# Kernel tuning notes

Measured on AMD Instinct MI355X. Metric: run time of the kernel, lower is better.

## Reference

```python
import jax, jax.numpy as jnp
import numpy as np

N_TV_ITER = 20      # fixed Chambolle iteration count (skimage early-stops via eps; fixed for jit)
TV_WEIGHT = 0.1


def _div(p):
    # negative adjoint of forward-difference gradient (skimage convention)
    d = -(p[0] + p[1])
    d = d.at[1:, :].add(p[0, :-1, :])
    d = d.at[:, 1:].add(p[1, :, :-1])
    return d


def tv_chambolle_2d(image):
    """skimage.restoration.denoise_tv_chambolle on a single 2D image, weight=0.1."""
    tau = 0.25  # 1 / (2 * ndim)

    def step(p, _):
        out = image + _div(p)
        gy = jnp.zeros_like(out).at[:-1, :].set(out[1:, :] - out[:-1, :])
        gx = jnp.zeros_like(out).at[:, :-1].set(out[:, 1:] - out[:, :-1])
        norm = jnp.sqrt(gy * gy + gx * gx)
        g = jnp.stack([gy, gx])
        p = (p - tau * g) / (1.0 + (tau / TV_WEIGHT) * norm)
        return p, None

    p0 = jnp.zeros((2,) + image.shape, image.dtype)
    p, _ = jax.lax.scan(step, p0, None, length=N_TV_ITER)
    return image + _div(p)


def tv_denoise(img):  # [B,C,H,W], vmapped over B*C (replaces the CPU python loop)
    B, C, H, W = img.shape
    out = jax.vmap(tv_chambolle_2d)(img.reshape(B * C, H, W))
    return out.reshape(B, C, H, W)


def conv(x, w, stride=1, groups=1):
    pad = w.shape[2] // 2  # 'same'-style padding for odd kernels, 0 for 1x1
    return jax.lax.conv_general_dilated(
        x, w, (stride, stride), [(pad, pad), (pad, pad)],
        dimension_numbers=('NCHW', 'OIHW', 'NCHW'),
        feature_group_count=groups)


def haar_ll(x):
    # one level of pywt wavedec2('haar') LL band: 0.5 * sum over each 2x2 block
    return 0.5 * (x[..., ::2, ::2] + x[..., ::2, 1::2] + x[..., 1::2, ::2] + x[..., 1::2, 1::2])


def backbone(x, stem_w, dw_pw):
    # stride-32, 1280-channel EfficientNet-B0-style feature extractor
    x = jax.nn.silu(conv(x, stem_w, stride=2))
    for dw, pw in dw_pw:
        x = jax.nn.silu(conv(x, dw, stride=2, groups=dw.shape[0]))
        x = jax.nn.silu(conv(x, pw))
    return x


def setup_inputs() -> dict:
    key = jax.random.key(0)
    ks = jax.random.split(key, 16)
    B, H, W = 4, 512, 512

    def w(k, o, i, kh, kw):
        return jax.random.normal(k, (o, i, kh, kw), jnp.float32) * (1.0 / np.sqrt(i * kh * kw))

    return {
        "img": jax.random.normal(ks[0], (B, 1, H, W), jnp.float32),
        "stem_w": w(ks[1], 32, 1, 3, 3),
        "dw1_w": w(ks[2], 32, 1, 3, 3),  "pw1_w": w(ks[3], 64, 32, 1, 1),
        "dw2_w": w(ks[4], 64, 1, 3, 3),  "pw2_w": w(ks[5], 128, 64, 1, 1),
        "dw3_w": w(ks[6], 128, 1, 3, 3), "pw3_w": w(ks[7], 256, 128, 1, 1),
        "dw4_w": w(ks[8], 256, 1, 3, 3), "pw4_w": w(ks[9], 512, 256, 1, 1),
        "head_w": w(ks[10], 1280, 512, 1, 1),
        "proj_w": w(ks[11], 64, 1280, 1, 1),
        "proj_b": jnp.zeros((64,), jnp.float32),
        "final_w": w(ks[12], 1, 64, 1, 1),
        "final_b": jnp.zeros((1,), jnp.float32),
    }


def reference(img, stem_w, dw1_w, pw1_w, dw2_w, pw2_w, dw3_w, pw3_w, dw4_w, pw4_w,
              head_w, proj_w, proj_b, final_w, final_b):
    B, C, H, W = img.shape
    x = tv_denoise(img)                                     # fused TV Chambolle
    x = backbone(x, stem_w, [(dw1_w, pw1_w), (dw2_w, pw2_w), (dw3_w, pw3_w), (dw4_w, pw4_w)])
    x = jax.nn.silu(conv(x, head_w))                        # [B,1280,H/32,W/32]
    x = conv(x, proj_w) + proj_b[None, :, None, None]       # [B,64,H/32,W/32]
    x = jax.image.resize(x, (B, 64, H, W), method='bilinear')  # align_corners=False semantics
    ll = haar_ll(haar_ll(x))                                # 2-level Haar LL: [B,64,H/4,W/4]
    out = conv(ll, final_w) + final_b[None, :, None, None]  # [B,1,H/4,W/4]
    return out
```

## Files before the change

kernel.cpp:

```cpp
#include <hip/hip_runtime.h>
#include <math.h>

constexpr int BATCH = 4;
constexpr int IMG_H = 512, IMG_W = 512;
constexpr int IMG_HW = IMG_H * IMG_W;
constexpr int PSTR = BATCH * IMG_HW;

constexpr size_t O_PA   = 0;
constexpr size_t O_PB   = O_PA + 2 * (size_t)PSTR;
constexpr size_t O_DEN  = O_PB + 2 * (size_t)PSTR;
constexpr size_t O_A1   = O_DEN + (size_t)PSTR;
constexpr size_t O_A2   = O_A1 + 8388608;
constexpr size_t O_WT1  = O_A2 + 2097152;
constexpr size_t O_WT2  = O_WT1 + 32 * 64;
constexpr size_t O_WT3  = O_WT2 + 64 * 128;
constexpr size_t O_WT4  = O_WT3 + 128 * 256;
constexpr size_t O_WTH  = O_WT4 + 256 * 512;
constexpr size_t O_WCOMB= O_WTH + 512 * 1280;
constexpr size_t O_BCOMB= O_WCOMB + 1280;
constexpr size_t O_S    = O_BCOMB + 4;
constexpr size_t WS_FLOATS = O_S + 1024;

__device__ __forceinline__ float silu_f(float x) {
    return x / (1.0f + expf(-x));
}
__device__ __forceinline__ int clampi(int v, int lo, int hi) {
    return v < lo ? lo : (v > hi ? hi : v);
}

template <int NST, bool FIRST, bool LAST>
__global__ __launch_bounds__(512) void tv_reg(const float* __restrict__ img,
                                              const float* __restrict__ pin,
                                              float* __restrict__ pout) {
    constexpr int ROWS = 7, NW = 8, HL = 10, TC = 44, TR = 32;
    __shared__ float bndP[512], bndO[512];
    const int tid = threadIdx.x;
    const int lane = tid & 63, w = tid >> 6;
    const int b = blockIdx.z;
    const int r0 = blockIdx.y * TR, c0 = blockIdx.x * TC;
    const int gj = c0 - HL + lane;
    const int gjc = clampi(gj, 0, 511);
    const int gib = r0 - HL + w * ROWS;
    const float* I = img + b * IMG_HW;
    const bool interior = (r0 - HL >= 1) && (r0 + NW * ROWS - HL <= 511) &&
                          (c0 - HL >= 1) && (c0 + 64 - HL <= 511);

    float rim[ROWS], rp0[ROWS], rp1[ROWS], ro[ROWS];
#pragma unroll
    for (int k = 0; k < ROWS; ++k) {
        int gi = clampi(gib + k, 0, 511);
        rim[k] = I[(gi << 9) + gjc];
    }
    if (!FIRST) {
        const float* P0 = pin + b * IMG_HW;
        const float* P1 = pin + PSTR + b * IMG_HW;
#pragma unroll
        for (int k = 0; k < ROWS; ++k) {
            int gi = clampi(gib + k, 0, 511);
            rp0[k] = P0[(gi << 9) + gjc];
            rp1[k] = P1[(gi << 9) + gjc];
        }
    }
    const bool gjpos = (gj > 0), gjlt = (gj < 511);

    int s0 = 0;
    if (FIRST) {
        bndO[tid] = rim[0];
        __syncthreads();
        float odn = (w < NW - 1) ? bndO[tid + 64] : 0.0f;
        if (interior) {
#pragma unroll
            for (int k = 0; k < ROWS; ++k) {
                float oR = __shfl_down(rim[k], 1);
                float od = (k < ROWS - 1) ? rim[k + 1] : odn;
                float gy = od - rim[k];
                float gx = oR - rim[k];
                float inv = 1.0f / (1.0f + 2.5f * sqrtf(gy * gy + gx * gx));
                rp0[k] = -0.25f * gy * inv;
                rp1[k] = -0.25f * gx * inv;
            }
        } else {
#pragma unroll
            for (int k = 0; k < ROWS; ++k) {
                float oR = __shfl_down(rim[k], 1);
                float od = (k < ROWS - 1) ? rim[k + 1] : odn;
                int gi = gib + k;
                float gy = (gi < 511) ? od - rim[k] : 0.0f;
                float gx = gjlt ? oR - rim[k] : 0.0f;
                float inv = 1.0f / (1.0f + 2.5f * sqrtf(gy * gy + gx * gx));
                rp0[k] = -0.25f * gy * inv;
                rp1[k] = -0.25f * gx * inv;
            }
        }
        s0 = 1;
    }

    for (int s = s0; s < NST; ++s) {
        __syncthreads();
        bndP[tid] = rp0[ROWS - 1];
        __syncthreads();
        float pup0 = (w > 0) ? bndP[tid - 64] : 0.0f;
        if (interior) {
#pragma unroll
            for (int k = 0; k < ROWS; ++k) {
                float p1l = __shfl_up(rp1[k], 1);
                float pup = (k > 0) ? rp0[k - 1] : pup0;
                ro[k] = rim[k] - rp0[k] - rp1[k] + pup + p1l;
            }
            bndO[tid] = ro[0];
            __syncthreads();
            float odn = (w < NW - 1) ? bndO[tid + 64] : 0.0f;
#pragma unroll
            for (int k = 0; k < ROWS; ++k) {
                float oR = __shfl_down(ro[k], 1);
                float od = (k < ROWS - 1) ? ro[k + 1] : odn;
                float gy = od - ro[k];
                float gx = oR - ro[k];
                float inv = 1.0f / (1.0f + 2.5f * sqrtf(gy * gy + gx * gx));
                rp0[k] = (rp0[k] - 0.25f * gy) * inv;
                rp1[k] = (rp1[k] - 0.25f * gx) * inv;
            }
        } else {
#pragma unroll
            for (int k = 0; k < ROWS; ++k) {
                float p1l = __shfl_up(rp1[k], 1);
                float o = rim[k] - rp0[k] - rp1[k];
                float pup = (k > 0) ? rp0[k - 1] : pup0;
                int gi = gib + k;
                if (gi > 0) o += pup;
                if (gjpos) o += p1l;
                ro[k] = o;
            }
            bndO[tid] = ro[0];
            __syncthreads();
            float odn = (w < NW - 1) ? bndO[tid + 64] : 0.0f;
#pragma unroll
            for (int k = 0; k < ROWS; ++k) {
                float oR = __shfl_down(ro[k], 1);
                float od = (k < ROWS - 1) ? ro[k + 1] : odn;
                int gi = gib + k;
                float gy = (gi < 511) ? od - ro[k] : 0.0f;
                float gx = gjlt ? oR - ro[k] : 0.0f;
                float inv = 1.0f / (1.0f + 2.5f * sqrtf(gy * gy + gx * gx));
                rp0[k] = (rp0[k] - 0.25f * gy) * inv;
                rp1[k] = (rp1[k] - 0.25f * gx) * inv;
            }
        }
    }

    const bool cst = (lane >= HL && lane < HL + TC && gj < 512);
    if (LAST) {
        __syncthreads();
        bndP[tid] = rp0[ROWS - 1];
        __syncthreads();
        float pup0 = (w > 0) ? bndP[tid - 64] : 0.0f;
        float* D = pout + b * IMG_HW;
#pragma unroll
        for (int k = 0; k < ROWS; ++k) {
            float p1l = __shfl_up(rp1[k], 1);
            int gi = gib + k;
            int rk = w * ROWS + k;
            float o = rim[k] - rp0[k] - rp1[k];
            float pup = (k > 0) ? rp0[k - 1] : pup0;
            if (gi > 0) o += pup;
            if (gjpos) o += p1l;
            if (rk >= HL && rk < HL + TR && cst) D[(gi << 9) + gj] = o;
        }
    } else {
        float* Q0 = pout + b * IMG_HW;
        float* Q1 = pout + PSTR + b * IMG_HW;
#pragma unroll
        for (int k = 0; k < ROWS; ++k) {
            int rk = w * ROWS + k;
            int gi = gib + k;
            if (rk >= HL && rk < HL + TR && cst) {
                Q0[(gi << 9) + gj] = rp0[k];
                Q1[(gi << 9) + gj] = rp1[k];
            }
        }
    }
}

__global__ __launch_bounds__(256) void stem_dw1_pw1(const float* __restrict__ den,
                                                    const float* __restrict__ stemw,
                                                    const float* __restrict__ dw1w,
                                                    const float* __restrict__ pw1T,
                                                    float* __restrict__ out) {
    __shared__ float sDen[35 * 36];
    __shared__ float sStem[8 * 323];
    __shared__ float sDw[32 * 64];
    __shared__ float sW[576];
    __shared__ __align__(16) float sWp[2048];
    const int tid = threadIdx.x;
    const int b = blockIdx.z;
    const int r0 = blockIdx.y * 32, c0 = blockIdx.x * 32;
    const float* D = den + b * IMG_HW;
    for (int e = tid; e < 576; e += 256) sW[e] = (e < 288) ? stemw[e] : dw1w[e - 288];
    for (int e = tid; e < 2048; e += 256) sWp[e] = pw1T[e];
    for (int e = tid; e < 35 * 35; e += 256) {
        int li = e / 35, lj = e % 35;
        int gi = r0 - 3 + li, gjj = c0 - 3 + lj;
        sDen[li * 36 + lj] = (gi >= 0 && gjj >= 0) ? D[(gi << 9) + gjj] : 0.0f;
    }
    __syncthreads();

    for (int g = 0; g < 4; ++g) {
        if (g) __syncthreads();
        for (int e = tid; e < 2312; e += 256) {
            int pos = e >> 3, cl = e & 7;
            int sy = pos / 17, sx = pos % 17;
            int c = 8 * g + cl;
            const float* wc = &sW[c * 9];
            const float* dbase = &sDen[(2 * sy) * 36 + 2 * sx];
            float a = 0.0f;
#pragma unroll
            for (int ky = 0; ky < 3; ++ky)
#pragma unroll
                for (int kx = 0; kx < 3; ++kx)
                    a = fmaf(wc[ky * 3 + kx], dbase[ky * 36 + kx], a);
            sStem[cl * 323 + sy * 19 + sx] = silu_f(a);
        }
        __syncthreads();
        for (int e = tid; e < 512; e += 256) {
            int cl = e >> 6, dy = (e >> 3) & 7, dx = e & 7;
            int c = 8 * g + cl;
            float acc = 0.0f;
#pragma unroll
            for (int ky = 0; ky < 3; ++ky)
#pragma unroll
                for (int kx = 0; kx < 3; ++kx) {
                    int sgy = (r0 >> 1) - 1 + 2 * dy + ky;
                    int sgx = (c0 >> 1) - 1 + 2 * dx + kx;
                    float v = (sgy >= 0 && sgx >= 0)
                        ? sStem[cl * 323 + (2 * dy + ky) * 19 + 2 * dx + kx] : 0.0f;
                    acc = fmaf(sW[288 + c * 9 + ky * 3 + kx], v, acc);
                }
            sDw[c * 64 + (dy << 3) + dx] = silu_f(acc);
        }
    }
    __syncthreads();

    const int px = tid & 63, oc0 = (tid >> 6) * 16;
    float acc[16];
#pragma unroll
    for (int j = 0; j < 16; ++j) acc[j] = 0.0f;
    for (int ic = 0; ic < 32; ++ic) {
        float v = sDw[ic * 64 + px];
        const float* wr = &sWp[ic * 64 + oc0];
#pragma unroll
        for (int q = 0; q < 4; ++q) {
            float4 w4 = *(const float4*)(wr + q * 4);
            acc[q * 4 + 0] = fmaf(v, w4.x, acc[q * 4 + 0]);
            acc[q * 4 + 1] = fmaf(v, w4.y, acc[q * 4 + 1]);
            acc[q * 4 + 2] = fmaf(v, w4.z, acc[q * 4 + 2]);
            acc[q * 4 + 3] = fmaf(v, w4.w, acc[q * 4 + 3]);
        }
    }
    const int gpos = ((r0 >> 2) + (px >> 3)) * 128 + (c0 >> 2) + (px & 7);
    float* ob = out + (size_t)b * 64 * 16384 + (size_t)oc0 * 16384 + gpos;
#pragma unroll
    for (int j = 0; j < 16; ++j) ob[(size_t)j * 16384] = silu_f(acc[j]);
}

template <int C, int HIN>
__global__ __launch_bounds__(256) void dw_kernel(const float* __restrict__ in,
                                                 const float* __restrict__ w,
                                                 float* __restrict__ out) {
    constexpr int HO = HIN / 2;
    int t = blockIdx.x * 256 + threadIdx.x;
    int x = t % HO;
    int y = (t / HO) % HO;
    int c = (t / (HO * HO)) % C;
    int b = t / (HO * HO * C);
    const float* I = in + ((size_t)(b * C + c)) * (HIN * HIN);
    const float* wc = w + c * 9;
    int iy = 2 * y - 1, ix = 2 * x - 1;
    float acc = 0.0f;
#pragma unroll
    for (int ky = 0; ky < 3; ++ky)
#pragma unroll
        for (int kx = 0; kx < 3; ++kx) {
            int yy = iy + ky, xx = ix + kx;
            float vv = (yy >= 0 && xx >= 0) ? I[yy * HIN + xx] : 0.0f;
            acc = fmaf(wc[ky * 3 + kx], vv, acc);
        }
    out[t] = silu_f(acc);
}

template <int C, int HIN>
__global__ __launch_bounds__(256) void dw_reduce2_kernel(const float* __restrict__ part,
                                                         const float* __restrict__ w,
                                                         float* __restrict__ out) {
    constexpr int HO = HIN / 2;
    int t = blockIdx.x * 256 + threadIdx.x;
    int x = t % HO;
    int y = (t / HO) % HO;
    int c = (t / (HO * HO)) % C;
    int b = t / (HO * HO * C);
    const float* Ia = part + ((size_t)(b * C + c)) * (HIN * HIN);
    const float* Ib = Ia + (size_t)BATCH * C * HIN * HIN;
    const float* wc = w + c * 9;
    int iy = 2 * y - 1, ix = 2 * x - 1;
    float acc = 0.0f;
#pragma unroll
    for (int ky = 0; ky < 3; ++ky)
#pragma unroll
        for (int kx = 0; kx < 3; ++kx) {
            int yy = iy + ky, xx = ix + kx;
            float vv = 0.0f;
            if (yy >= 0 && xx >= 0) {
                int o = yy * HIN + xx;
                vv = silu_f(Ia[o] + Ib[o]);
            }
            acc = fmaf(wc[ky * 3 + kx], vv, acc);
        }
    out[t] = silu_f(acc);
}

template <int ICT, int NSIN, int NSPLIT, int OC, bool SILU>
__global__ __launch_bounds__(256) void pw_gemm(const float* __restrict__ in,
                                               const float* __restrict__ wT,
                                               float* __restrict__ out,
                                               int HW) {
    constexpr int KC = 32, TP = 64, TOC = 64, OPT = 4, PPT = 4;
    constexpr int KS = ICT / NSPLIT;
    constexpr int NC = KS / KC;
    constexpr int NOG = TOC / OPT;
    constexpr int PV4 = KC * TP / 4 / 256;
    constexpr int WV4 = KC * TOC / 4 / 256;
    static_assert(KS % KC == 0, "split");
    __shared__ __align__(16) float sPx[2][KC * TP];
    __shared__ __align__(16) float sW[2][KC * TOC];
    const int tid = threadIdx.x;
    const int zb = blockIdx.z;
    const int b = zb / NSPLIT, ks = zb % NSPLIT;
    const int p0 = blockIdx.x * TP;
    const int oc0 = blockIdx.y * TOC;
    const int ocg = tid % NOG, pxg = tid / NOG;
    const size_t instride = (size_t)BATCH * ICT * HW;
    const float* gin0 = in + ((size_t)b * ICT + ks * KS) * HW + p0;
    const float* gw0  = wT + ((size_t)(ks * KS)) * OC + oc0;

    float4 rp[PV4], rw[WV4];
    auto load_chunk = [&](int cc) {
        const float* gin = gin0 + (size_t)cc * KC * HW;
#pragma unroll
        for (int i = 0; i < PV4; ++i) {
            int e = tid + i * 256;
            int row = e / (TP / 4), col = e % (TP / 4);
            const float* base = gin + (size_t)row * HW + col * 4;
            float4 a = *(const float4*)base;
#pragma unroll
            for (int s = 1; s < NSIN; ++s) {
                float4 t4 = *(const float4*)(base + (size_t)s * instride);
                a.x += t4.x; a.y += t4.y; a.z += t4.z; a.w += t4.w;
            }
            if (NSIN > 1) {
                a.x = silu_f(a.x); a.y = silu_f(a.y);
                a.z = silu_f(a.z); a.w = silu_f(a.w);
            }
            rp[i] = a;
        }
        const float* gw = gw0 + (size_t)cc * KC * OC;
#pragma unroll
        for (int i = 0; i < WV4; ++i) {
            int e = tid + i * 256;
            int row = e / (TOC / 4), col = e % (TOC / 4);
            rw[i] = *(const float4*)(gw + (size_t)row * OC + col * 4);
        }
    };
    auto store_chunk = [&](int buf) {
#pragma unroll
        for (int i = 0; i < PV4; ++i) ((float4*)sPx[buf])[tid + i * 256] = rp[i];
#pragma unroll
        for (int i = 0; i < WV4; ++i) ((float4*)sW[buf])[tid + i * 256] = rw[i];
    };

    float acc[OPT][PPT];
#pragma unroll
    for (int o = 0; o < OPT; ++o)
#pragma unroll
        for (int p = 0; p < PPT; ++p) acc[o][p] = 0.0f;

    load_chunk(0);
    store_chunk(0);
    __syncthreads();
    for (int cc = 0; cc < NC; ++cc) {
        if (cc + 1 < NC) load_chunk(cc + 1);
        const int buf = cc & 1;
#pragma unroll 4
        for (int k = 0; k < KC; ++k) {
            float4 pv = *(const float4*)&sPx[buf][k * TP + pxg * PPT];
            float4 wv = *(const float4*)&sW[buf][k * TOC + ocg * OPT];
            float w0 = wv.x, w1 = wv.y, w2 = wv.z, w3 = wv.w;
            acc[0][0] = fmaf(pv.x, w0, acc[0][0]);
            acc[0][1] = fmaf(pv.y, w0, acc[0][1]);
            acc[0][2] = fmaf(pv.z, w0, acc[0][2]);
            acc[0][3] = fmaf(pv.w, w0, acc[0][3]);
            acc[1][0] = fmaf(pv.x, w1, acc[1][0]);
            acc[1][1] = fmaf(pv.y, w1, acc[1][1]);
            acc[1][2] = fmaf(pv.z, w1, acc[1][2]);
            acc[1][3] = fmaf(pv.w, w1, acc[1][3]);
            acc[2][0] = fmaf(pv.x, w2, acc[2][0]);
            acc[2][1] = fmaf(pv.y, w2, acc[2][1]);
            acc[2][2] = fmaf(pv.z, w2, acc[2][2]);
            acc[2][3] = fmaf(pv.w, w2, acc[2][3]);
            acc[3][0] = fmaf(pv.x, w3, acc[3][0]);
            acc[3][1] = fmaf(pv.y, w3, acc[3][1]);
            acc[3][2] = fmaf(pv.z, w3, acc[3][2]);
            acc[3][3] = fmaf(pv.w, w3, acc[3][3]);
        }
        if (cc + 1 < NC) {
            store_chunk((cc + 1) & 1);
            __syncthreads();
        }
    }

    float* ob;
    if (NSPLIT == 1)
        ob = out + ((size_t)(b * OC + oc0 + ocg * OPT)) * HW + p0 + pxg * PPT;
    else
        ob = out + (((size_t)(ks * BATCH + b)) * OC + oc0 + ocg * OPT) * HW + p0 + pxg * PPT;
#pragma unroll
    for (int o = 0; o < OPT; ++o) {
        float4 r;
        r.x = SILU ? silu_f(acc[o][0]) : acc[o][0];
        r.y = SILU ? silu_f(acc[o][1]) : acc[o][1];
        r.z = SILU ? silu_f(acc[o][2]) : acc[o][2];
        r.w = SILU ? silu_f(acc[o][3]) : acc[o][3];
        *(float4*)(ob + (size_t)o * HW) = r;
    }
}

__global__ __launch_bounds__(256) void prep_kernel(const float* __restrict__ pw1,
                                                   const float* __restrict__ pw2,
                                                   const float* __restrict__ pw3,
                                                   const float* __restrict__ pw4,
                                                   const float* __restrict__ headw,
                                                   const float* __restrict__ projw,
                                                   const float* __restrict__ projb,
                                                   const float* __restrict__ finalw,
                                                   const float* __restrict__ finalb,
                                                   float* __restrict__ ws) {
    int t = blockIdx.x * 256 + threadIdx.x;
    if (t < 2048) {
        int e = t; int ic = e >> 6, oc = e & 63;
        ws[O_WT1 + e] = pw1[oc * 32 + ic];
    } else if (t < 10240) {
        int e = t - 2048; int ic = e >> 7, oc = e & 127;
        ws[O_WT2 + e] = pw2[oc * 64 + ic];
    } else if (t < 43008) {
        int e = t - 10240; int ic = e >> 8, oc = e & 255;
        ws[O_WT3 + e] = pw3[oc * 128 + ic];
    } else if (t < 174080) {
        int e = t - 43008; int ic = e >> 9, oc = e & 511;
        ws[O_WT4 + e] = pw4[oc * 256 + ic];
    } else if (t < 829440) {
        int e = t - 174080; int ic = e / 1280, oc = e % 1280;
        ws[O_WTH + e] = headw[oc * 512 + ic];
    } else if (t < 830720) {
        int k = t - 829440;
        float a = 0.0f;
        for (int ch = 0; ch < 64; ++ch) a = fmaf(finalw[ch], projw[ch * 1280 + k], a);
        ws[O_WCOMB + k] = a;
    } else if (t == 830720) {
        float a = 0.0f;
        for (int ch = 0; ch < 64; ++ch) a = fmaf(finalw[ch], projb[ch], a);
        ws[O_BCOMB] = a;
    }
}

__global__ __launch_bounds__(256) void tail_head(const float* __restrict__ part,
                                                 const float* __restrict__ wcomb,
                                                 const float* __restrict__ bcomb,
                                                 float* __restrict__ s) {
    __shared__ float red[256];
    constexpr size_t PS = (size_t)4 * 1280 * 256;
    int b = blockIdx.x >> 4;
    int px0 = (blockIdx.x & 15) << 4;
    int px = threadIdx.x & 15, kg = threadIdx.x >> 4;
    const float* h0 = part + (size_t)b * 1280 * 256 + px0 + px;
    float acc = 0.0f;
    int k0 = kg * 80;
    for (int k = k0; k < k0 + 80; ++k) {
        size_t off = (size_t)k * 256;
        float v = silu_f(h0[off] + h0[off + PS] + h0[off + 2 * PS] + h0[off + 3 * PS]);
        acc = fmaf(wcomb[k], v, acc);
    }
    red[threadIdx.x] = acc;
    __syncthreads();
    if (threadIdx.x < 16) {
        float a = bcomb[0];
#pragma unroll
        for (int g = 0; g < 16; ++g) a += red[g * 16 + threadIdx.x];
        s[b * 256 + px0 + threadIdx.x] = a;
    }
}

__global__ __launch_bounds__(256) void resize_haar(const float* __restrict__ s,
                                                   const float* __restrict__ finalb,
                                                   float* __restrict__ out) {
    int t = blockIdx.x * 256 + threadIdx.x;
    int c = t & 127, r = (t >> 7) & 127, b = t >> 14;
    const float* S = s + b * 256;
    float acc = 0.0f;
#pragma unroll
    for (int j = 0; j < 4; ++j) {
        float sy = ((4 * r + j) + 0.5f) * (1.0f / 32.0f) - 0.5f;
        int y0 = (int)floorf(sy);
        float fy = sy - (float)y0;
        int ya = y0 < 0 ? 0 : y0;
        int yb = (y0 + 1) > 15 ? 15 : (y0 + 1);
#pragma unroll
        for (int i = 0; i < 4; ++i) {
            float sx = ((4 * c + i) + 0.5f) * (1.0f / 32.0f) - 0.5f;
            int x0 = (int)floorf(sx);
            float fx = sx - (float)x0;
            int xa = x0 < 0 ? 0 : x0;
            int xb = (x0 + 1) > 15 ? 15 : (x0 + 1);
            float v0 = S[ya * 16 + xa] * (1.0f - fx) + S[ya * 16 + xb] * fx;
            float v1 = S[yb * 16 + xa] * (1.0f - fx) + S[yb * 16 + xb] * fx;
            acc += v0 * (1.0f - fy) + v1 * fy;
        }
    }
    out[t] = 0.25f * acc + finalb[0];
}

extern "C" void kernel_launch(void* const* d_in, const int* in_sizes, int n_in,
                              void* d_out, int out_size, void* d_ws, size_t ws_size,
                              hipStream_t stream) {
    if (ws_size < WS_FLOATS * sizeof(float)) return;

    const float* img    = (const float*)d_in[0];
    const float* stem_w = (const float*)d_in[1];
    const float* dw1_w  = (const float*)d_in[2];
    const float* pw1_w  = (const float*)d_in[3];
    const float* dw2_w  = (const float*)d_in[4];
    const float* pw2_w  = (const float*)d_in[5];
    const float* dw3_w  = (const float*)d_in[6];
    const float* pw3_w  = (const float*)d_in[7];
    const float* dw4_w  = (const float*)d_in[8];
    const float* pw4_w  = (const float*)d_in[9];
    const float* head_w = (const float*)d_in[10];
    const float* proj_w = (const float*)d_in[11];
    const float* proj_b = (const float*)d_in[12];
    const float* final_w= (const float*)d_in[13];
    const float* final_b= (const float*)d_in[14];
    float* ws  = (float*)d_ws;
    float* out = (float*)d_out;

    prep_kernel<<<3246, 256, 0, stream>>>(pw1_w, pw2_w, pw3_w, pw4_w, head_w,
                                          proj_w, proj_b, final_w, final_b, ws);

    dim3 tvg(12, 16, 4);
    tv_reg<10, true,  false><<<tvg, 512, 0, stream>>>(img, img,       ws + O_PA);
    tv_reg<10, false, true ><<<tvg, 512, 0, stream>>>(img, ws + O_PA, ws + O_DEN);

    stem_dw1_pw1<<<dim3(16, 16, 4), 256, 0, stream>>>(ws + O_DEN, stem_w, dw1_w,
                                                      ws + O_WT1, ws + O_A1);

    dw_kernel<64, 128><<<4096, 256, 0, stream>>>(ws + O_A1, dw2_w, ws + O_A2);
    pw_gemm<64, 1, 2, 128, false><<<dim3(64, 2, 8), 256, 0, stream>>>(ws + O_A2, ws + O_WT2, ws + O_PA, 4096);

    dw_reduce2_kernel<128, 64><<<2048, 256, 0, stream>>>(ws + O_PA, dw3_w, ws + O_A1);
    pw_gemm<128, 1, 2, 256, false><<<dim3(16, 4, 8), 256, 0, stream>>>(ws + O_A1, ws + O_WT3, ws + O_PA, 1024);

    dw_reduce2_kernel<256, 32><<<1024, 256, 0, stream>>>(ws + O_PA, dw4_w, ws + O_A2);
    pw_gemm<256, 1, 4, 512, false><<<dim3(4, 8, 16), 256, 0, stream>>>(ws + O_A2, ws + O_WT4, ws + O_PA, 256);

    pw_gemm<512, 4, 4, 1280, false><<<dim3(4, 20, 16), 256, 0, stream>>>(ws + O_PA, ws + O_WTH, ws + O_A1, 256);
    tail_head<<<64, 256, 0, stream>>>(ws + O_A1, ws + O_WCOMB, ws + O_BCOMB, ws + O_S);

    resize_haar<<<256, 256, 0, stream>>>(ws + O_S, final_b, out);
}
```

Before: 293.9 us.

## Use fast hardware math intrinsics, drop redundant barriers, tile weight transposes

Replaces IEEE division, sqrt and expf in the TV Chambolle loop and silu with AMD hardware rcp/sqrt/exp2 builtins. Removes two __syncthreads calls in the TV iteration loop that are redundant given the barriers already between shared-buffer reuse. Rewrites the weight-preparation kernel as a 32x32 shared-memory tiled transpose with far fewer blocks, so both reads and writes are coalesced. The fast intrinsics lose a little accuracy relative to the IEEE-accurate versions.

```diff
diff --git a/kernel.cpp b/kernel.cpp
--- a/kernel.cpp
+++ b/kernel.cpp
@@ -21,8 +21,11 @@
 constexpr size_t O_S    = O_BCOMB + 4;
 constexpr size_t WS_FLOATS = O_S + 1024;
 
+__device__ __forceinline__ float fast_rcp(float x) { return __builtin_amdgcn_rcpf(x); }
+__device__ __forceinline__ float fast_sqrt(float x) { return __builtin_amdgcn_sqrtf(x); }
 __device__ __forceinline__ float silu_f(float x) {
-    return x / (1.0f + expf(-x));
+    float e = __builtin_amdgcn_exp2f(-1.44269504088896f * x);
+    return x * fast_rcp(1.0f + e);
 }
 __device__ __forceinline__ int clampi(int v, int lo, int hi) {
     return v < lo ? lo : (v > hi ? hi : v);
@@ -75,7 +78,7 @@
                 float od = (k < ROWS - 1) ? rim[k + 1] : odn;
                 float gy = od - rim[k];
                 float gx = oR - rim[k];
-                float inv = 1.0f / (1.0f + 2.5f * sqrtf(gy * gy + gx * gx));
+                float inv = fast_rcp(fmaf(2.5f, fast_sqrt(fmaf(gy, gy, gx * gx)), 1.0f));
                 rp0[k] = -0.25f * gy * inv;
                 rp1[k] = -0.25f * gx * inv;
             }
@@ -87,7 +90,7 @@
                 int gi = gib + k;
                 float gy = (gi < 511) ? od - rim[k] : 0.0f;
                 float gx = gjlt ? oR - rim[k] : 0.0f;
-                float inv = 1.0f / (1.0f + 2.5f * sqrtf(gy * gy + gx * gx));
+                float inv = fast_rcp(fmaf(2.5f, fast_sqrt(fmaf(gy, gy, gx * gx)), 1.0f));
                 rp0[k] = -0.25f * gy * inv;
                 rp1[k] = -0.25f * gx * inv;
             }
@@ -96,7 +99,6 @@
     }
 
     for (int s = s0; s < NST; ++s) {
-        __syncthreads();
         bndP[tid] = rp0[ROWS - 1];
         __syncthreads();
         float pup0 = (w > 0) ? bndP[tid - 64] : 0.0f;
@@ -116,7 +118,7 @@
                 float od = (k < ROWS - 1) ? ro[k + 1] : odn;
                 float gy = od - ro[k];
                 float gx = oR - ro[k];
-                float inv = 1.0f / (1.0f + 2.5f * sqrtf(gy * gy + gx * gx));
+                float inv = fast_rcp(fmaf(2.5f, fast_sqrt(fmaf(gy, gy, gx * gx)), 1.0f));
                 rp0[k] = (rp0[k] - 0.25f * gy) * inv;
                 rp1[k] = (rp1[k] - 0.25f * gx) * inv;
             }
@@ -141,7 +143,7 @@
                 int gi = gib + k;
                 float gy = (gi < 511) ? od - ro[k] : 0.0f;
                 float gx = gjlt ? oR - ro[k] : 0.0f;
-                float inv = 1.0f / (1.0f + 2.5f * sqrtf(gy * gy + gx * gx));
+                float inv = fast_rcp(fmaf(2.5f, fast_sqrt(fmaf(gy, gy, gx * gx)), 1.0f));
                 rp0[k] = (rp0[k] - 0.25f * gy) * inv;
                 rp1[k] = (rp1[k] - 0.25f * gx) * inv;
             }
@@ -150,7 +152,6 @@
 
     const bool cst = (lane >= HL && lane < HL + TC && gj < 512);
     if (LAST) {
-        __syncthreads();
         bndP[tid] = rp0[ROWS - 1];
         __syncthreads();
         float pup0 = (w > 0) ? bndP[tid - 64] : 0.0f;
@@ -442,32 +443,54 @@
                                                    const float* __restrict__ finalw,
                                                    const float* __restrict__ finalb,
                                                    float* __restrict__ ws) {
-    int t = blockIdx.x * 256 + threadIdx.x;
-    if (t < 2048) {
-        int e = t; int ic = e >> 6, oc = e & 63;
-        ws[O_WT1 + e] = pw1[oc * 32 + ic];
-    } else if (t < 10240) {
-        int e = t - 2048; int ic = e >> 7, oc = e & 127;
-        ws[O_WT2 + e] = pw2[oc * 64 + ic];
-    } else if (t < 43008) {
-        int e = t - 10240; int ic = e >> 8, oc = e & 255;
-        ws[O_WT3 + e] = pw3[oc * 128 + ic];
-    } else if (t < 174080) {
-        int e = t - 43008; int ic = e >> 9, oc = e & 511;
-        ws[O_WT4 + e] = pw4[oc * 256 + ic];
-    } else if (t < 829440) {
-        int e = t - 174080; int ic = e / 1280, oc = e % 1280;
-        ws[O_WTH + e] = headw[oc * 512 + ic];
-    } else if (t < 830720) {
-        int k = t - 829440;
-        float a = 0.0f;
-        for (int ch = 0; ch < 64; ++ch) a = fmaf(finalw[ch], projw[ch * 1280 + k], a);
-        ws[O_WCOMB + k] = a;
-    } else if (t == 830720) {
-        float a = 0.0f;
-        for (int ch = 0; ch < 64; ++ch) a = fmaf(finalw[ch], projb[ch], a);
-        ws[O_BCOMB] = a;
-    }
+    __shared__ float t[32][33];
+    const int bx = blockIdx.x;
+    const float* src;
+    float* dst;
+    int R, C, tr, tc;
+    if (bx < 640) {
+        src = headw; dst = ws + O_WTH; R = 1280; C = 512;
+        tr = bx >> 4; tc = bx & 15;
+    } else if (bx < 768) {
+        int e = bx - 640;
+        src = pw4; dst = ws + O_WT4; R = 512; C = 256;
+        tr = e >> 3; tc = e & 7;
+    } else if (bx < 800) {
+        int e = bx - 768;
+        src = pw3; dst = ws + O_WT3; R = 256; C = 128;
+        tr = e >> 2; tc = e & 3;
+    } else if (bx < 808) {
+        int e = bx - 800;
+        src = pw2; dst = ws + O_WT2; R = 128; C = 64;
+        tr = e >> 1; tc = e & 1;
+    } else if (bx < 810) {
+        int e = bx - 808;
+        src = pw1; dst = ws + O_WT1; R = 64; C = 32;
+        tr = e; tc = 0;
+    } else if (bx < 815) {
+        int k = (bx - 810) * 256 + threadIdx.x;
+        if (k < 1280) {
+            float a = 0.0f;
+            for (int ch = 0; ch < 64; ++ch) a = fmaf(finalw[ch], projw[ch * 1280 + k], a);
+            ws[O_WCOMB + k] = a;
+        }
+        return;
+    } else {
+        if (threadIdx.x == 0) {
+            float a = 0.0f;
+            for (int ch = 0; ch < 64; ++ch) a = fmaf(finalw[ch], projb[ch], a);
+            ws[O_BCOMB] = a;
+        }
+        return;
+    }
+    const int tx = threadIdx.x & 31, ty = threadIdx.x >> 5;
+#pragma unroll
+    for (int j = 0; j < 4; ++j)
+        t[ty + j * 8][tx] = src[(size_t)(tr * 32 + ty + j * 8) * C + tc * 32 + tx];
+    __syncthreads();
+#pragma unroll
+    for (int j = 0; j < 4; ++j)
+        dst[(size_t)(tc * 32 + ty + j * 8) * R + tr * 32 + tx] = t[tx][ty + j * 8];
 }
 
 __global__ __launch_bounds__(256) void tail_head(const float* __restrict__ part,
@@ -549,8 +572,8 @@
     float* ws  = (float*)d_ws;
     float* out = (float*)d_out;
 
-    prep_kernel<<<3246, 256, 0, stream>>>(pw1_w, pw2_w, pw3_w, pw4_w, head_w,
-                                          proj_w, proj_b, final_w, final_b, ws);
+    prep_kernel<<<816, 256, 0, stream>>>(pw1_w, pw2_w, pw3_w, pw4_w, head_w,
+                                         proj_w, proj_b, final_w, final_b, ws);
 
     dim3 tvg(12, 16, 4);
     tv_reg<10, true,  false><<<tvg, 512, 0, stream>>>(img, img,       ws + O_PA);
```

Result: faster. 252.3 us (-14.2%).
